# Optimization experiments

Measured on AMD Instinct MI355X. Metric: run time of the kernel, lower is better.

Reference implementation:

```python
import jax, jax.numpy as jnp
import numpy as np

B, N, D, H = 4, 1024, 1024, 16
DH = D // H
NEG_BIG = -2.0**32 + 1.0  # padding value from the torch code


def setup_inputs() -> dict:
    key = jax.random.key(0)
    ks = jax.random.split(key, 12)
    inp = {
        "x": jax.random.normal(ks[0], (B, N, D), dtype=jnp.float32),
        "key_padding_mask": jnp.zeros((B, N), dtype=bool),  # True = padded
        # attention projections (nn.Linear, bias=False): y = x @ W.T
        "Wq": jax.random.normal(ks[1], (D, D), dtype=jnp.float32) * (D ** -0.5),
        "Wk": jax.random.normal(ks[2], (D, D), dtype=jnp.float32) * (D ** -0.5),
        "Wv": jax.random.normal(ks[3], (D, D), dtype=jnp.float32) * (D ** -0.5),
        # FFN
        "W1": jax.random.normal(ks[4], (D, D), dtype=jnp.float32) * (D ** -0.5),
        "b1": jnp.zeros((D,), dtype=jnp.float32),
        "W2": jax.random.normal(ks[5], (D, D), dtype=jnp.float32) * (D ** -0.5),
        "b2": jnp.zeros((D,), dtype=jnp.float32),
        # MaskedLayerNorm params
        "g1": jnp.ones((D,), dtype=jnp.float32),
        "beta1": jnp.zeros((D,), dtype=jnp.float32),
        "g2": jnp.ones((D,), dtype=jnp.float32),
        "beta2": jnp.zeros((D,), dtype=jnp.float32),
    }
    return inp


def masked_layer_norm(x, scale, bias, eps=1e-5):
    mean = jnp.mean(x, axis=-1, keepdims=True)
    var = jnp.mean(jnp.square(x - mean), axis=-1, keepdims=True)
    return (x - mean) * jax.lax.rsqrt(var + eps) * scale + bias


def _to_heads(t):
    # torch: cat(split(t, DH, dim=2), dim=0) -> head-major [H*B, N, DH]
    b, n, d = t.shape
    return t.reshape(b, n, H, DH).transpose(2, 0, 1, 3).reshape(H * b, n, DH)


def _from_heads(t, b):
    # torch: cat(split(t, B, dim=0), dim=2) -> [B, N, D]
    hb, n, dh = t.shape
    return t.reshape(H, b, n, dh).transpose(1, 2, 0, 3).reshape(b, n, H * dh)


def attention(x, key_padding_mask, Wq, Wk, Wv):
    b, n, d = x.shape
    Q = _to_heads(x @ Wq.T)  # (H*B, N, DH)
    K = _to_heads(x @ Wk.T)
    V = _to_heads(x @ Wv.T)

    scores = jnp.einsum("znd,zmd->znm", Q, K) / (DH ** 0.5)  # (H*B, N, N)

    # key masks: sign of sum|K| over feature dim, broadcast over query axis
    key_masks = jnp.sign(jnp.sum(jnp.abs(K), axis=-1))  # (H*B, N)
    scores = jnp.where(key_masks[:, None, :] == 0, jnp.full_like(scores, NEG_BIG), scores)

    # temporal mask, direction == FORWARD: mask[i, j] = (j > i)
    idx = jnp.arange(n)
    attn_mask = idx[None, :] > idx[:, None]  # sw_row > sw_col with ij meshgrid
    scores = scores + (1.0 - attn_mask.astype(scores.dtype)) * -10000.0

    # NOTE: original code calls F.softmax(outputs) with no dim on a 3D tensor;
    # torch's implicit-dim rule selects dim=0 for ndim==3. Replicated faithfully.
    attn = jax.nn.softmax(scores, axis=0)

    query_masks = jnp.sign(jnp.sum(jnp.abs(Q), axis=-1))  # (H*B, N)
    attn = attn * query_masks[:, :, None]
    # dropout p=0.0 -> identity

    out = jnp.einsum("znm,zmd->znd", attn, V)  # (H*B, N, DH)
    out = _from_heads(out, b)  # (B, N, D)
    out = out * (~key_padding_mask)[:, :, None].astype(out.dtype)
    return out


def reference(x, key_padding_mask, Wq, Wk, Wv, W1, b1, W2, b2, g1, beta1, g2, beta2):
    attn_out = attention(x, key_padding_mask, Wq, Wk, Wv)
    h = masked_layer_norm(x + attn_out, g1, beta1)  # layer_norm1
    ff = jax.nn.relu(h @ W1.T + b1) @ W2.T + b2  # fc (dropout p=0)
    valid = (~key_padding_mask)[:, :, None].astype(ff.dtype)
    ff = ff * valid
    out = masked_layer_norm(ff + h, g2, beta2)  # layer_norm2
    out = out * valid
    return out
```

## Files before the change

### kernel.cpp

```cpp
#include <hip/hip_runtime.h>
#include <math.h>

typedef unsigned short u16;
typedef unsigned char  u8;
typedef unsigned int   u32;
typedef __attribute__((ext_vector_type(8))) short bf16x8;
typedef __attribute__((ext_vector_type(4))) float f32x4;

#define NSEQ   1024
#define DMODEL 1024
#define ZTOT   64
#define LOG2E  1.4426950408889634f

typedef const __attribute__((address_space(1))) void* gp1;
typedef __attribute__((address_space(3))) void* lp3;

__device__ __forceinline__ void gload16(const void* g, void* l) {
    __builtin_amdgcn_global_load_lds((gp1)g, (lp3)l, 16, 0, 0);
}

__device__ __forceinline__ u16 f2bf(float f) {
    u32 u = __builtin_bit_cast(u32, f);
    return (u16)((u + 0x7FFFu + ((u >> 16) & 1u)) >> 16);
}

__device__ __forceinline__ u32 cvt_pk_bf16(float a, float b) {
    u32 r;
    asm("v_cvt_pk_bf16_f32 %0, %1, %2" : "=v"(r) : "v"(a), "v"(b));
    return r;
}

__launch_bounds__(256)
__global__ void cvt_bf16(const float* __restrict__ in, u16* __restrict__ out) {
    int i = (blockIdx.x * 256 + threadIdx.x) * 4;
    float4 v = *(const float4*)(in + i);
    uint2 o;
    o.x = cvt_pk_bf16(v.x, v.y);
    o.y = cvt_pk_bf16(v.z, v.w);
    *(uint2*)(out + i) = o;
}

struct P5 { const float* in[5]; u16* out[5]; };
__launch_bounds__(256)
__global__ void cvt_bf16_5(P5 p) {
    int which = blockIdx.x >> 10;
    int blk   = blockIdx.x & 1023;
    int i = (blk * 256 + threadIdx.x) * 4;
    float4 v = *(const float4*)(p.in[which] + i);
    uint2 o;
    o.x = cvt_pk_bf16(v.x, v.y);
    o.y = cvt_pk_bf16(v.z, v.w);
    *(uint2*)(p.out[which] + i) = o;
}

__launch_bounds__(256)
__global__ void rowmask2_bf(const u16* __restrict__ Kh, const u16* __restrict__ Qh,
                            float* __restrict__ km, float* __restrict__ qm) {
    int b = blockIdx.x;
    const u16* T = (b < 256) ? Kh : Qh;
    float* o = (b < 256) ? km : qm;
    int r = (b & 255) * 256 + threadIdx.x;
    const uint4* p = (const uint4*)(T + (size_t)r * 64);
    u32 acc = 0;
    #pragma unroll
    for (int i = 0; i < 8; i++) {
        uint4 q = p[i];
        acc |= (q.x | q.y | q.z | q.w) & 0x7fff7fffu;
    }
    o[r] = acc ? 1.f : 0.f;
}

__launch_bounds__(256)
__global__ void vt_km(u16* __restrict__ Vt, const float* __restrict__ km) {
    int idx = blockIdx.x * 256 + threadIdx.x;
    int e0 = idx * 8;
    int z = e0 >> 16;
    int tok = e0 & 1023;
    float4 ka = *(const float4*)(km + z * 1024 + tok);
    float4 kb = *(const float4*)(km + z * 1024 + tok + 4);
    uint4 v = *(uint4*)(Vt + e0);
    u32 m;
    m = (ka.x != 0.f ? 0x0000FFFFu : 0u) | (ka.y != 0.f ? 0xFFFF0000u : 0u); v.x &= m;
    m = (ka.z != 0.f ? 0x0000FFFFu : 0u) | (ka.w != 0.f ? 0xFFFF0000u : 0u); v.y &= m;
    m = (kb.x != 0.f ? 0x0000FFFFu : 0u) | (kb.y != 0.f ? 0xFFFF0000u : 0u); v.z &= m;
    m = (kb.z != 0.f ? 0x0000FFFFu : 0u) | (kb.w != 0.f ? 0xFFFF0000u : 0u); v.w &= m;
    *(uint4*)(Vt + e0) = v;
}

__launch_bounds__(256)
__global__ void gemm_qkv(const u16* __restrict__ A,
                         const u16* __restrict__ Wq, const u16* __restrict__ Wk,
                         const u16* __restrict__ Wv,
                         u16* __restrict__ Qh, u16* __restrict__ Kh, u16* __restrict__ Vt)
{
    __shared__ __align__(16) u16 lA[2][128 * 32];
    __shared__ __align__(16) u16 lB[2][128 * 32];
    const int tid = threadIdx.x, lane = tid & 63, w = tid >> 6;
    const int frow = lane & 15, koct = lane >> 4;
    const int sel = blockIdx.x >> 3;
    const int col0 = (blockIdx.x & 7) * 128, row0 = blockIdx.y * 128;
    const u16* B = (sel == 0) ? Wq : (sel == 1) ? Wk : Wv;
    const int wrow = (w >> 1) * 64, wcol = (w & 1) * 64;
    f32x4 acc[4][4] = {};

    auto stage = [&](int buf, int k0) {
        #pragma unroll
        for (int i = 0; i < 2; i++) {
            int p = tid + i * 256;
            int row = p >> 2, sl = p & 3, ssl = sl ^ ((row >> 1) & 3);
            gload16(A + (size_t)(row0 + row) * 1024 + k0 + ssl * 8, (char*)lA[buf] + p * 16);
        }
        #pragma unroll
        for (int i = 0; i < 2; i++) {
            int p = tid + i * 256;
            int row = p >> 2, sl = p & 3, ssl = sl ^ ((row >> 1) & 3);
            gload16(B + (size_t)(col0 + row) * 1024 + k0 + ssl * 8, (char*)lB[buf] + p * 16);
        }
    };

    stage(0, 0);
    __syncthreads();
    int buf = 0;
    for (int k0 = 0; k0 < 1024; k0 += 32) {
        if (k0 + 32 < 1024) stage(buf ^ 1, k0 + 32);
        __builtin_amdgcn_s_setprio(1);
        bf16x8 af[4], bf[4];
        #pragma unroll
        for (int i = 0; i < 4; i++) {
            int r = wrow + i * 16 + frow;
            int sl = koct ^ ((r >> 1) & 3);
            af[i] = *(const bf16x8*)((const char*)lA[buf] + r * 64 + sl * 16);
        }
        #pragma unroll
        for (int j = 0; j < 4; j++) {
            int r = wcol + j * 16 + frow;
            int sl = koct ^ ((r >> 1) & 3);
            bf[j] = *(const bf16x8*)((const char*)lB[buf] + r * 64 + sl * 16);
        }
        #pragma unroll
        for (int i = 0; i < 4; i++)
            #pragma unroll
            for (int j = 0; j < 4; j++)
                acc[i][j] = __builtin_amdgcn_mfma_f32_16x16x32_bf16(af[i], bf[j], acc[i][j], 0, 0, 0);
        __builtin_amdgcn_s_setprio(0);
        __syncthreads();
        buf ^= 1;
    }

    if (sel < 2) {
        const float scale = (sel == 0) ? 0.125f * LOG2E : 1.0f;
        u16* outp = (sel == 0) ? Qh : Kh;
        #pragma unroll
        for (int i = 0; i < 4; i++)
            #pragma unroll
            for (int j = 0; j < 4; j++)
                #pragma unroll
                for (int q = 0; q < 4; q++) {
                    int r = row0 + wrow + i * 16 + koct * 4 + q;
                    int c = col0 + wcol + j * 16 + frow;
                    float v = acc[i][j][q] * scale;
                    outp[(size_t)((c >> 6) * 4 + (r >> 10)) * 65536 +
                         (size_t)(r & 1023) * 64 + (c & 63)] = f2bf(v);
                }
    } else {
        #pragma unroll
        for (int i = 0; i < 4; i++) {
            int r0 = row0 + wrow + i * 16 + koct * 4;
            #pragma unroll
            for (int j = 0; j < 4; j++) {
                int c = col0 + wcol + j * 16 + frow;
                int z = (c >> 6) * 4 + (r0 >> 10);
                uint2 pk;
                pk.x = cvt_pk_bf16(acc[i][j][0], acc[i][j][1]);
                pk.y = cvt_pk_bf16(acc[i][j][2], acc[i][j][3]);
                *(uint2*)(Vt + (size_t)z * 65536 + (size_t)(c & 63) * 1024 + (r0 & 1023)) = pk;
            }
        }
    }
}

template <int MODE>
__launch_bounds__(256)
__global__ void gemm_bt(const u16* __restrict__ A, const u16* __restrict__ B,
                        const float* __restrict__ bias, void* __restrict__ outp)
{
    __shared__ __align__(16) u16 lA[2][128 * 64];
    __shared__ __align__(16) u16 lB[2][64 * 64];
    const int tid = threadIdx.x, lane = tid & 63, w = tid >> 6;
    const int frow = lane & 15, koct = lane >> 4;
    const int col0 = blockIdx.x * 64, row0 = blockIdx.y * 128;
    const int wrow = (w >> 1) * 64, wcol = (w & 1) * 32;
    f32x4 acc[4][2] = {};

    auto stage = [&](int buf, int k0) {
        #pragma unroll
        for (int i = 0; i < 4; i++) {
            int p = tid + i * 256;
            int row = p >> 3, sl = p & 7, ssl = sl ^ (row & 7);
            gload16(A + (size_t)(row0 + row) * 1024 + k0 + ssl * 8, (char*)lA[buf] + p * 16);
        }
        #pragma unroll
        for (int i = 0; i < 2; i++) {
            int p = tid + i * 256;
            int row = p >> 3, sl = p & 7, ssl = sl ^ (row & 7);
            gload16(B + (size_t)(col0 + row) * 1024 + k0 + ssl * 8, (char*)lB[buf] + p * 16);
        }
    };

    stage(0, 0);
    __syncthreads();
    int buf = 0;
    for (int k0 = 0; k0 < 1024; k0 += 64) {
        if (k0 + 64 < 1024) stage(buf ^ 1, k0 + 64);
        __builtin_amdgcn_s_setprio(1);
        #pragma unroll
        for (int ks = 0; ks < 2; ks++) {
            bf16x8 af[4], bf2[2];
            #pragma unroll
            for (int i = 0; i < 4; i++) {
                int r = wrow + i * 16 + frow;
                int sl = (ks * 4 + koct) ^ (r & 7);
                af[i] = *(const bf16x8*)((const char*)lA[buf] + r * 128 + sl * 16);
            }
            #pragma unroll
            for (int j = 0; j < 2; j++) {
                int r = wcol + j * 16 + frow;
                int sl = (ks * 4 + koct) ^ (r & 7);
                bf2[j] = *(const bf16x8*)((const char*)lB[buf] + r * 128 + sl * 16);
            }
            #pragma unroll
            for (int i = 0; i < 4; i++)
                #pragma unroll
                for (int j = 0; j < 2; j++)
                    acc[i][j] = __builtin_amdgcn_mfma_f32_16x16x32_bf16(af[i], bf2[j], acc[i][j], 0, 0, 0);
        }
        __builtin_amdgcn_s_setprio(0);
        __syncthreads();
        buf ^= 1;
    }

    #pragma unroll
    for (int i = 0; i < 4; i++)
        #pragma unroll
        for (int j = 0; j < 2; j++)
            #pragma unroll
            for (int q = 0; q < 4; q++) {
                int r = row0 + wrow + i * 16 + koct * 4 + q;
                int c = col0 + wcol + j * 16 + frow;
                float v = acc[i][j][q] + bias[c];
                if constexpr (MODE == 2) {
                    v = fmaxf(v, 0.f);
                    ((u16*)outp)[(size_t)r * 1024 + c] = f2bf(v);
                } else {
                    ((float*)outp)[(size_t)r * 1024 + c] = v;
                }
            }
}

__launch_bounds__(256)
__global__ void attn_pass1(const u16* __restrict__ Qh, const u16* __restrict__ Kh,
                           const float* __restrict__ km, float* __restrict__ partial)
{
    const int bid = blockIdx.x;
    const int mtzg = (bid & 7) * 8 + ((bid >> 3) & 7);
    const int m0 = (mtzg & 15) * 64, zg = mtzg >> 4;
    const int n0 = (bid >> 6) * 64;

    __shared__ __align__(16) u16 lQ[2][64 * 64];
    __shared__ __align__(16) u16 lK[2][64 * 64];
    const int tid = threadIdx.x, lane = tid & 63, w = tid >> 6;
    const int frow = lane & 15, koct = lane >> 4;
    const int wn = (w >> 1) * 32, wm = (w & 1) * 32;
    f32x4 ssum[2][2] = {};

    auto stage = [&](int buf, int z) {
        #pragma unroll
        for (int i = 0; i < 2; i++) {
            int p = tid + i * 256;
            int row = p >> 3, sl = p & 7, ssl = sl ^ (row & 7);
            gload16(Qh + (size_t)(z * NSEQ + n0 + row) * 64 + ssl * 8, (char*)lQ[buf] + p * 16);
            gload16(Kh + (size_t)(z * NSEQ + m0 + row) * 64 + ssl * 8, (char*)lK[buf] + p * 16);
        }
    };

    const int z0 = zg * 16;
    stage(0, z0);
    __syncthreads();
    int buf = 0;
    for (int zi = 0; zi < 16; zi++) {
        const int z = z0 + zi;
        if (zi < 15) stage(buf ^ 1, z + 1);
        f32x4 km4[2];
        #pragma unroll
        for (int j = 0; j < 2; j++)
            km4[j] = *(const f32x4*)(km + z * NSEQ + m0 + wm + j * 16 + koct * 4);
        f32x4 s[2][2] = {};
        __builtin_amdgcn_s_setprio(1);
        #pragma unroll
        for (int ks = 0; ks < 2; ks++) {
            bf16x8 a[2], b2[2];
            #pragma unroll
            for (int i = 0; i < 2; i++) {
                int r = wn + i * 16 + frow;
                int sl = (ks * 4 + koct) ^ (r & 7);
                a[i] = *(const bf16x8*)((const char*)lQ[buf] + r * 128 + sl * 16);
            }
            #pragma unroll
            for (int j = 0; j < 2; j++) {
                int r = wm + j * 16 + frow;
                int sl = (ks * 4 + koct) ^ (r & 7);
                b2[j] = *(const bf16x8*)((const char*)lK[buf] + r * 128 + sl * 16);
            }
            #pragma unroll
            for (int i = 0; i < 2; i++)
                #pragma unroll
                for (int j = 0; j < 2; j++)
                    s[i][j] = __builtin_amdgcn_mfma_f32_16x16x32_bf16(b2[j], a[i], s[i][j], 0, 0, 0);
        }
        __builtin_amdgcn_s_setprio(0);
        #pragma unroll
        for (int j = 0; j < 2; j++)
            #pragma unroll
            for (int i = 0; i < 2; i++)
                #pragma unroll
                for (int q = 0; q < 4; q++)
                    ssum[i][j][q] += __builtin_amdgcn_exp2f(s[i][j][q]) * km4[j][q];
        __syncthreads();
        buf ^= 1;
    }
    #pragma unroll
    for (int i = 0; i < 2; i++)
        #pragma unroll
        for (int j = 0; j < 2; j++) {
            int ng = n0 + wn + i * 16 + frow;
            int mg = m0 + wm + j * 16 + koct * 4;
            *(f32x4*)(partial + (size_t)zg * 1048576 + (size_t)ng * NSEQ + mg) = ssum[i][j];
        }
}

__launch_bounds__(256)
__global__ void sum_inv(const float* __restrict__ p, float* __restrict__ invS) {
    int i = (blockIdx.x * 256 + threadIdx.x) * 4;
    float4 a = *(const float4*)(p + i);
    float4 b = *(const float4*)(p + 1048576 + i);
    float4 c = *(const float4*)(p + 2097152 + i);
    float4 d = *(const float4*)(p + 3145728 + i);
    float4 r;
    float s;
    s = a.x + b.x + c.x + d.x; r.x = s > 0.f ? 1.f / s : 0.f;
    s = a.y + b.y + c.y + d.y; r.y = s > 0.f ? 1.f / s : 0.f;
    s = a.z + b.z + c.z + d.z; r.z = s > 0.f ? 1.f / s : 0.f;
    s = a.w + b.w + c.w + d.w; r.w = s > 0.f ? 1.f / s : 0.f;
    *(float4*)(invS + i) = r;
}

__launch_bounds__(256)
__global__ void attn_pass2(const u16* __restrict__ Qh, const u16* __restrict__ Kh,
                           const u16* __restrict__ Vt,
                           const float* __restrict__ qm, const float* __restrict__ invS,
                           const u8* __restrict__ pad, float* __restrict__ attn)
{
    const int bid = blockIdx.x;
    const int z  = (bid & 7) * 8 + ((bid >> 3) & 7);
    const int n0 = (bid >> 6) * 64;

    __shared__ __align__(16) u16 lK[2][64 * 64];
    __shared__ __align__(16) u16 lV[2][64 * 64];
    __shared__ __align__(16) u16 lP[64 * 64];
    const int tid = threadIdx.x, lane = tid & 63, w = tid >> 6;
    const int frow = lane & 15, koct = lane >> 4;
    const int hh = z >> 2, bb = z & 3;
    const int wrow = w * 16;
    const int nl_row = wrow + frow;
    const size_t inv_base = (size_t)(n0 + nl_row) * NSEQ;

    bf16x8 aq[2];
    #pragma unroll
    for (int ks = 0; ks < 2; ks++)
        aq[ks] = *(const bf16x8*)(Qh + (size_t)(z * NSEQ + n0 + nl_row) * 64 + ks * 32 + koct * 8);

    auto stage = [&](int buf, int m0) {
        #pragma unroll
        for (int i = 0; i < 2; i++) {
            int p = tid + i * 256;
            int row = p >> 3, sl = p & 7, ssl = sl ^ (row & 7);
            gload16(Kh + (size_t)(z * NSEQ + m0 + row) * 64 + ssl * 8, (char*)lK[buf] + p * 16);
            gload16(Vt + (size_t)z * 65536 + (size_t)row * 1024 + m0 + ssl * 8, (char*)lV[buf] + p * 16);
        }
    };

    f32x4 oacc[4] = {};
    f32x4 iv[4];
    #pragma unroll
    for (int j = 0; j < 4; j++)
        iv[j] = *(const f32x4*)(invS + inv_base + j * 16 + koct * 4);
    stage(0, 0);
    __syncthreads();
    int buf = 0;

    for (int mt = 0; mt < 16; mt++) {
        const int m0 = mt * 64;
        if (mt < 15) stage(buf ^ 1, m0 + 64);
        f32x4 ivn[4];
        if (mt < 15) {
            #pragma unroll
            for (int j = 0; j < 4; j++)
                ivn[j] = *(const f32x4*)(invS + inv_base + m0 + 64 + j * 16 + koct * 4);
        }
        f32x4 s[4] = {};
        __builtin_amdgcn_s_setprio(1);
        #pragma unroll
        for (int ks = 0; ks < 2; ks++) {
            bf16x8 kb[4];
            #pragma unroll
            for (int j = 0; j < 4; j++) {
                int r = j * 16 + frow;
                int sl = (ks * 4 + koct) ^ (r & 7);
                kb[j] = *(const bf16x8*)((const char*)lK[buf] + r * 128 + sl * 16);
            }
            #pragma unroll
            for (int j = 0; j < 4; j++)
                s[j] = __builtin_amdgcn_mfma_f32_16x16x32_bf16(kb[j], aq[ks], s[j], 0, 0, 0);
        }
        __builtin_amdgcn_s_setprio(0);
        #pragma unroll
        for (int j = 0; j < 4; j++) {
            float p0 = __builtin_amdgcn_exp2f(s[j][0]) * iv[j][0];
            float p1 = __builtin_amdgcn_exp2f(s[j][1]) * iv[j][1];
            float p2 = __builtin_amdgcn_exp2f(s[j][2]) * iv[j][2];
            float p3 = __builtin_amdgcn_exp2f(s[j][3]) * iv[j][3];
            uint2 pk;
            pk.x = cvt_pk_bf16(p0, p1);
            pk.y = cvt_pk_bf16(p2, p3);
            int slot = (j * 2 + (koct >> 1)) ^ (nl_row & 7);
            *(uint2*)((char*)lP + nl_row * 128 + slot * 16 + (koct & 1) * 8) = pk;
        }
        __builtin_amdgcn_s_setprio(1);
        #pragma unroll
        for (int ks = 0; ks < 2; ks++) {
            int sl = (ks * 4 + koct) ^ (nl_row & 7);
            bf16x8 pa = *(const bf16x8*)((const char*)lP + nl_row * 128 + sl * 16);
            bf16x8 vb[4];
            #pragma unroll
            for (int dj = 0; dj < 4; dj++) {
                int rr = dj * 16 + frow;
                int sv = (ks * 4 + koct) ^ (rr & 7);
                vb[dj] = *(const bf16x8*)((const char*)lV[buf] + rr * 128 + sv * 16);
            }
            #pragma unroll
            for (int dj = 0; dj < 4; dj++)
                oacc[dj] = __builtin_amdgcn_mfma_f32_16x16x32_bf16(pa, vb[dj], oacc[dj], 0, 0, 0);
        }
        __builtin_amdgcn_s_setprio(0);
        __syncthreads();
        buf ^= 1;
        #pragma unroll
        for (int j = 0; j < 4; j++) iv[j] = ivn[j];
    }

    #pragma unroll
    for (int q = 0; q < 4; q++) {
        int ns = n0 + wrow + koct * 4 + q;
        float f = qm[z * NSEQ + ns] * (pad[bb * NSEQ + ns] ? 0.f : 1.f);
        #pragma unroll
        for (int dj = 0; dj < 4; dj++) {
            int d = dj * 16 + frow;
            attn[(size_t)(bb * NSEQ + ns) * DMODEL + hh * 64 + d] = oacc[dj][q] * f;
        }
    }
}

__launch_bounds__(256)
__global__ void ln_kernel(const float* __restrict__ A, const float* __restrict__ Bv,
                          const float* __restrict__ g, const float* __restrict__ beta,
                          const u8* __restrict__ pad, int mode,
                          float* __restrict__ out, u16* __restrict__ outb)
{
    const int row = blockIdx.x, tid = threadIdx.x;
    const int lane = tid & 63, wv = tid >> 6;
    const float valid = pad[row] ? 0.f : 1.f;
    __shared__ float red[4];

    float4 va = *(const float4*)(A + (size_t)row * 1024 + tid * 4);
    float4 vb = *(const float4*)(Bv + (size_t)row * 1024 + tid * 4);
    float v[4];
    if (mode == 0) {
        v[0] = va.x + vb.x; v[1] = va.y + vb.y; v[2] = va.z + vb.z; v[3] = va.w + vb.w;
    } else {
        v[0] = va.x * valid + vb.x; v[1] = va.y * valid + vb.y;
        v[2] = va.z * valid + vb.z; v[3] = va.w * valid + vb.w;
    }
    float s = v[0] + v[1] + v[2] + v[3];
    #pragma unroll
    for (int off = 32; off > 0; off >>= 1) s += __shfl_down(s, off, 64);
    if (lane == 0) red[wv] = s;
    __syncthreads();
    float mean = (red[0] + red[1] + red[2] + red[3]) * (1.f / 1024.f);
    float sq = 0.f;
    #pragma unroll
    for (int k = 0; k < 4; k++) { float d = v[k] - mean; sq += d * d; }
    __syncthreads();
    #pragma unroll
    for (int off = 32; off > 0; off >>= 1) sq += __shfl_down(sq, off, 64);
    if (lane == 0) red[wv] = sq;
    __syncthreads();
    float var = (red[0] + red[1] + red[2] + red[3]) * (1.f / 1024.f);
    float rstd = rsqrtf(var + 1e-5f);
    float osc = (mode == 0) ? 1.f : valid;
    #pragma unroll
    for (int k = 0; k < 4; k++) {
        int c = tid * 4 + k;
        float o = ((v[k] - mean) * rstd * g[c] + beta[c]) * osc;
        out[(size_t)row * 1024 + c] = o;
        if (outb) outb[(size_t)row * 1024 + c] = f2bf(o);
    }
}

extern "C" void kernel_launch(void* const* d_in, const int* in_sizes, int n_in,
                              void* d_out, int out_size, void* d_ws, size_t ws_size,
                              hipStream_t stream)
{
    const float* x   = (const float*)d_in[0];
    const u8*    pad = (const u8*)d_in[1];
    const float* Wq  = (const float*)d_in[2];
    const float* Wk  = (const float*)d_in[3];
    const float* Wv  = (const float*)d_in[4];
    const float* W1  = (const float*)d_in[5];
    const float* b1  = (const float*)d_in[6];
    const float* W2  = (const float*)d_in[7];
    const float* b2  = (const float*)d_in[8];
    const float* g1  = (const float*)d_in[9];
    const float* be1 = (const float*)d_in[10];
    const float* g2  = (const float*)d_in[11];
    const float* be2 = (const float*)d_in[12];
    float* out = (float*)d_out;

    u16* xb   = (u16*)d_ws;
    u16* Wqb  = xb   + 4194304;
    u16* Wkb  = Wqb  + 1048576;
    u16* Wvb  = Wkb  + 1048576;
    u16* W1b  = Wvb  + 1048576;
    u16* W2b  = W1b  + 1048576;
    u16* Qh   = W2b  + 1048576;
    u16* Kh   = Qh   + 4194304;
    u16* Vt   = Kh   + 4194304;
    u16* hb   = Vt   + 4194304;
    u16* ff1b = hb   + 4194304;
    float* km      = (float*)(ff1b + 4194304);
    float* qm      = km      + 65536;
    float* partial = qm      + 65536;
    float* invS    = partial + 4194304;
    float* h       = invS    + 1048576;

    cvt_bf16<<<4096, 256, 0, stream>>>(x, xb);
    P5 p5;
    p5.in[0] = Wq; p5.in[1] = Wk; p5.in[2] = Wv; p5.in[3] = W1; p5.in[4] = W2;
    p5.out[0] = Wqb; p5.out[1] = Wkb; p5.out[2] = Wvb; p5.out[3] = W1b; p5.out[4] = W2b;
    cvt_bf16_5<<<5120, 256, 0, stream>>>(p5);

    gemm_qkv<<<dim3(24, 32), 256, 0, stream>>>(xb, Wqb, Wkb, Wvb, Qh, Kh, Vt);

    rowmask2_bf<<<512, 256, 0, stream>>>(Kh, Qh, km, qm);
    vt_km<<<4096, 256, 0, stream>>>(Vt, km);

    attn_pass1<<<1024, 256, 0, stream>>>(Qh, Kh, km, partial);
    sum_inv<<<1024, 256, 0, stream>>>(partial, invS);
    attn_pass2<<<1024, 256, 0, stream>>>(Qh, Kh, Vt, qm, invS, pad, out);

    ln_kernel<<<4096, 256, 0, stream>>>(x, out, g1, be1, pad, 0, h, hb);

    gemm_bt<2><<<dim3(16, 32), 256, 0, stream>>>(hb,   W1b, b1, ff1b);
    gemm_bt<3><<<dim3(16, 32), 256, 0, stream>>>(ff1b, W2b, b2, out);

    ln_kernel<<<4096, 256, 0, stream>>>(out, h, g2, be2, pad, 1, out, nullptr);
}
```

Measured before the change: 200.2 us.

## Store intermediate activations in bf16 and merge conversion kernels

Attention output, the FFN second GEMM output and the first layernorm result are now stored as bf16 instead of fp32. The second layernorm reads the bf16 h residual rather than a separate fp32 copy. The two fp32-to-bf16 conversion launches are merged into one kernel, and the layernorm stores are vectorized. This is meant to cut global memory traffic in the memory-bound elementwise stages and save one launch, at the cost of extra rounding error in the residual path.

```diff
diff --git a/kernel.cpp b/kernel.cpp
--- a/kernel.cpp
+++ b/kernel.cpp
@@ -24,33 +24,37 @@
     return (u16)((u + 0x7FFFu + ((u >> 16) & 1u)) >> 16);
 }
 
+__device__ __forceinline__ float bf2f(u32 lo16) {
+    u32 t = lo16 << 16;
+    return __builtin_bit_cast(float, t);
+}
+
 __device__ __forceinline__ u32 cvt_pk_bf16(float a, float b) {
     u32 r;
     asm("v_cvt_pk_bf16_f32 %0, %1, %2" : "=v"(r) : "v"(a), "v"(b));
     return r;
 }
 
-__launch_bounds__(256)
-__global__ void cvt_bf16(const float* __restrict__ in, u16* __restrict__ out) {
-    int i = (blockIdx.x * 256 + threadIdx.x) * 4;
+struct P5 { const float* in[5]; u16* out[5]; };
+__launch_bounds__(256)
+__global__ void cvt_all(const float* __restrict__ x, u16* __restrict__ xb, P5 p) {
+    int bid = blockIdx.x;
+    const float* in;
+    u16* out;
+    int blk;
+    if (bid < 4096) { in = x; out = xb; blk = bid; }
+    else {
+        int which = (bid - 4096) >> 10;
+        blk = bid & 1023;
+        in = p.in[which];
+        out = p.out[which];
+    }
+    int i = (blk * 256 + threadIdx.x) * 4;
     float4 v = *(const float4*)(in + i);
     uint2 o;
     o.x = cvt_pk_bf16(v.x, v.y);
     o.y = cvt_pk_bf16(v.z, v.w);
     *(uint2*)(out + i) = o;
-}
-
-struct P5 { const float* in[5]; u16* out[5]; };
-__launch_bounds__(256)
-__global__ void cvt_bf16_5(P5 p) {
-    int which = blockIdx.x >> 10;
-    int blk   = blockIdx.x & 1023;
-    int i = (blk * 256 + threadIdx.x) * 4;
-    float4 v = *(const float4*)(p.in[which] + i);
-    uint2 o;
-    o.x = cvt_pk_bf16(v.x, v.y);
-    o.y = cvt_pk_bf16(v.z, v.w);
-    *(uint2*)(p.out[which] + i) = o;
 }
 
 __launch_bounds__(256)
@@ -182,7 +186,7 @@
 template <int MODE>
 __launch_bounds__(256)
 __global__ void gemm_bt(const u16* __restrict__ A, const u16* __restrict__ B,
-                        const float* __restrict__ bias, void* __restrict__ outp)
+                        const float* __restrict__ bias, u16* __restrict__ outp)
 {
     __shared__ __align__(16) u16 lA[2][128 * 64];
     __shared__ __align__(16) u16 lB[2][64 * 64];
@@ -248,12 +252,8 @@
                 int r = row0 + wrow + i * 16 + koct * 4 + q;
                 int c = col0 + wcol + j * 16 + frow;
                 float v = acc[i][j][q] + bias[c];
-                if constexpr (MODE == 2) {
-                    v = fmaxf(v, 0.f);
-                    ((u16*)outp)[(size_t)r * 1024 + c] = f2bf(v);
-                } else {
-                    ((float*)outp)[(size_t)r * 1024 + c] = v;
-                }
+                if constexpr (MODE == 2) v = fmaxf(v, 0.f);
+                outp[(size_t)r * 1024 + c] = f2bf(v);
             }
 }
 
@@ -358,7 +358,7 @@
 __global__ void attn_pass2(const u16* __restrict__ Qh, const u16* __restrict__ Kh,
                            const u16* __restrict__ Vt,
                            const float* __restrict__ qm, const float* __restrict__ invS,
-                           const u8* __restrict__ pad, float* __restrict__ attn)
+                           const u8* __restrict__ pad, u16* __restrict__ attn)
 {
     const int bid = blockIdx.x;
     const int z  = (bid & 7) * 8 + ((bid >> 3) & 7);
@@ -465,30 +465,38 @@
         #pragma unroll
         for (int dj = 0; dj < 4; dj++) {
             int d = dj * 16 + frow;
-            attn[(size_t)(bb * NSEQ + ns) * DMODEL + hh * 64 + d] = oacc[dj][q] * f;
-        }
-    }
-}
-
-__launch_bounds__(256)
-__global__ void ln_kernel(const float* __restrict__ A, const float* __restrict__ Bv,
+            attn[(size_t)(bb * NSEQ + ns) * DMODEL + hh * 64 + d] = f2bf(oacc[dj][q] * f);
+        }
+    }
+}
+
+template <int MODE>
+__launch_bounds__(256)
+__global__ void ln_kernel(const void* __restrict__ Ap, const void* __restrict__ Bp,
                           const float* __restrict__ g, const float* __restrict__ beta,
-                          const u8* __restrict__ pad, int mode,
-                          float* __restrict__ out, u16* __restrict__ outb)
+                          const u8* __restrict__ pad,
+                          float* __restrict__ outf, u16* __restrict__ outb)
 {
     const int row = blockIdx.x, tid = threadIdx.x;
     const int lane = tid & 63, wv = tid >> 6;
     const float valid = pad[row] ? 0.f : 1.f;
     __shared__ float red[4];
 
-    float4 va = *(const float4*)(A + (size_t)row * 1024 + tid * 4);
-    float4 vb = *(const float4*)(Bv + (size_t)row * 1024 + tid * 4);
     float v[4];
-    if (mode == 0) {
-        v[0] = va.x + vb.x; v[1] = va.y + vb.y; v[2] = va.z + vb.z; v[3] = va.w + vb.w;
+    if constexpr (MODE == 0) {
+        float4 va = *(const float4*)((const float*)Ap + (size_t)row * 1024 + tid * 4);
+        uint2 bbv = *(const uint2*)((const u16*)Bp + (size_t)row * 1024 + tid * 4);
+        v[0] = va.x + bf2f(bbv.x & 0xFFFFu);
+        v[1] = va.y + bf2f(bbv.x >> 16);
+        v[2] = va.z + bf2f(bbv.y & 0xFFFFu);
+        v[3] = va.w + bf2f(bbv.y >> 16);
     } else {
-        v[0] = va.x * valid + vb.x; v[1] = va.y * valid + vb.y;
-        v[2] = va.z * valid + vb.z; v[3] = va.w * valid + vb.w;
+        uint2 aav = *(const uint2*)((const u16*)Ap + (size_t)row * 1024 + tid * 4);
+        uint2 bbv = *(const uint2*)((const u16*)Bp + (size_t)row * 1024 + tid * 4);
+        v[0] = bf2f(aav.x & 0xFFFFu) * valid + bf2f(bbv.x & 0xFFFFu);
+        v[1] = bf2f(aav.x >> 16)     * valid + bf2f(bbv.x >> 16);
+        v[2] = bf2f(aav.y & 0xFFFFu) * valid + bf2f(bbv.y & 0xFFFFu);
+        v[3] = bf2f(aav.y >> 16)     * valid + bf2f(bbv.y >> 16);
     }
     float s = v[0] + v[1] + v[2] + v[3];
     #pragma unroll
@@ -506,13 +514,23 @@
     __syncthreads();
     float var = (red[0] + red[1] + red[2] + red[3]) * (1.f / 1024.f);
     float rstd = rsqrtf(var + 1e-5f);
-    float osc = (mode == 0) ? 1.f : valid;
-    #pragma unroll
-    for (int k = 0; k < 4; k++) {
-        int c = tid * 4 + k;
-        float o = ((v[k] - mean) * rstd * g[c] + beta[c]) * osc;
-        out[(size_t)row * 1024 + c] = o;
-        if (outb) outb[(size_t)row * 1024 + c] = f2bf(o);
+
+    if constexpr (MODE == 0) {
+        uint2 o;
+        float o0 = (v[0] - mean) * rstd * g[tid * 4 + 0] + beta[tid * 4 + 0];
+        float o1 = (v[1] - mean) * rstd * g[tid * 4 + 1] + beta[tid * 4 + 1];
+        float o2 = (v[2] - mean) * rstd * g[tid * 4 + 2] + beta[tid * 4 + 2];
+        float o3 = (v[3] - mean) * rstd * g[tid * 4 + 3] + beta[tid * 4 + 3];
+        o.x = cvt_pk_bf16(o0, o1);
+        o.y = cvt_pk_bf16(o2, o3);
+        *(uint2*)(outb + (size_t)row * 1024 + tid * 4) = o;
+    } else {
+        float4 o;
+        o.x = ((v[0] - mean) * rstd * g[tid * 4 + 0] + beta[tid * 4 + 0]) * valid;
+        o.y = ((v[1] - mean) * rstd * g[tid * 4 + 1] + beta[tid * 4 + 1]) * valid;
+        o.z = ((v[2] - mean) * rstd * g[tid * 4 + 2] + beta[tid * 4 + 2]) * valid;
+        o.w = ((v[3] - mean) * rstd * g[tid * 4 + 3] + beta[tid * 4 + 3]) * valid;
+        *(float4*)(outf + (size_t)row * 1024 + tid * 4) = o;
     }
 }
 
@@ -535,28 +553,28 @@
     const float* be2 = (const float*)d_in[12];
     float* out = (float*)d_out;
 
-    u16* xb   = (u16*)d_ws;
-    u16* Wqb  = xb   + 4194304;
-    u16* Wkb  = Wqb  + 1048576;
-    u16* Wvb  = Wkb  + 1048576;
-    u16* W1b  = Wvb  + 1048576;
-    u16* W2b  = W1b  + 1048576;
-    u16* Qh   = W2b  + 1048576;
-    u16* Kh   = Qh   + 4194304;
-    u16* Vt   = Kh   + 4194304;
-    u16* hb   = Vt   + 4194304;
-    u16* ff1b = hb   + 4194304;
-    float* km      = (float*)(ff1b + 4194304);
+    u16* xb    = (u16*)d_ws;
+    u16* Wqb   = xb    + 4194304;
+    u16* Wkb   = Wqb   + 1048576;
+    u16* Wvb   = Wkb   + 1048576;
+    u16* W1b   = Wvb   + 1048576;
+    u16* W2b   = W1b   + 1048576;
+    u16* Qh    = W2b   + 1048576;
+    u16* Kh    = Qh    + 4194304;
+    u16* Vt    = Kh    + 4194304;
+    u16* hb    = Vt    + 4194304;
+    u16* ff1b  = hb    + 4194304;
+    u16* ffb   = ff1b  + 4194304;
+    u16* attnb = ffb   + 4194304;
+    float* km      = (float*)(attnb + 4194304);
     float* qm      = km      + 65536;
     float* partial = qm      + 65536;
     float* invS    = partial + 4194304;
-    float* h       = invS    + 1048576;
-
-    cvt_bf16<<<4096, 256, 0, stream>>>(x, xb);
+
     P5 p5;
     p5.in[0] = Wq; p5.in[1] = Wk; p5.in[2] = Wv; p5.in[3] = W1; p5.in[4] = W2;
     p5.out[0] = Wqb; p5.out[1] = Wkb; p5.out[2] = Wvb; p5.out[3] = W1b; p5.out[4] = W2b;
-    cvt_bf16_5<<<5120, 256, 0, stream>>>(p5);
+    cvt_all<<<9216, 256, 0, stream>>>(x, xb, p5);
 
     gemm_qkv<<<dim3(24, 32), 256, 0, stream>>>(xb, Wqb, Wkb, Wvb, Qh, Kh, Vt);
 
@@ -565,12 +583,12 @@
 
     attn_pass1<<<1024, 256, 0, stream>>>(Qh, Kh, km, partial);
     sum_inv<<<1024, 256, 0, stream>>>(partial, invS);
-    attn_pass2<<<1024, 256, 0, stream>>>(Qh, Kh, Vt, qm, invS, pad, out);
-
-    ln_kernel<<<4096, 256, 0, stream>>>(x, out, g1, be1, pad, 0, h, hb);
+    attn_pass2<<<1024, 256, 0, stream>>>(Qh, Kh, Vt, qm, invS, pad, attnb);
+
+    ln_kernel<0><<<4096, 256, 0, stream>>>(x, attnb, g1, be1, pad, nullptr, hb);
 
     gemm_bt<2><<<dim3(16, 32), 256, 0, stream>>>(hb,   W1b, b1, ff1b);
-    gemm_bt<3><<<dim3(16, 32), 256, 0, stream>>>(ff1b, W2b, b2, out);
-
-    ln_kernel<<<4096, 256, 0, stream>>>(out, h, g2, be2, pad, 1, out, nullptr);
-}
+    gemm_bt<3><<<dim3(16, 32), 256, 0, stream>>>(ff1b, W2b, b2, ffb);
+
+    ln_kernel<1><<<4096, 256, 0, stream>>>(ffb, hb, g2, be2, pad, out, nullptr);
+}
```

Result: faster. 177.2 us (-11.5%).
